# Kernel tuning notes

Measured on AMD Instinct MI355X. Metric: run time of the kernel, lower is better.

The kernel has to match this reference:

```python
import jax, jax.numpy as jnp
import numpy as np

B, S, H, KVH, D, HID = 2, 2048, 32, 8, 128, 4096
WINDOW = 512
EPS = 1e-5
SCALE = D ** -0.5
NEG = jnp.finfo(jnp.float32).min


def cohere_layernorm(x, w):
    # true LayerNorm (mean-subtracting), fp32 compute, weight, no bias
    xf = x.astype(jnp.float32)
    mu = jnp.mean(xf, axis=-1, keepdims=True)
    var = jnp.mean((xf - mu) ** 2, axis=-1, keepdims=True)
    return (w.astype(jnp.float32) * (xf - mu) * jax.lax.rsqrt(var + EPS)).astype(x.dtype)


def rotate_half_interleaved(x):
    # interleaved pairs: (x0,x1,x2,x3,...) -> (-x1,x0,-x3,x2,...)
    x1 = x[..., ::2]
    x2 = x[..., 1::2]
    return jnp.stack([-x2, x1], axis=-1).reshape(x.shape)


def setup_inputs() -> dict:
    key = jax.random.key(0)
    ks = jax.random.split(key, 6)
    hidden_states = jax.random.normal(ks[0], (B, S, HID), jnp.float32)
    position_ids = jnp.broadcast_to(jnp.arange(S, dtype=jnp.int32), (B, S))
    # rotary table with interleave-repeated frequencies (Cohere style)
    inv_freq = 1.0 / (10000.0 ** (jnp.arange(0, D, 2, dtype=jnp.float32) / D))
    freqs = jnp.arange(S, dtype=jnp.float32)[:, None] * inv_freq[None, :]  # [S, D/2]
    emb = jnp.repeat(freqs, 2, axis=-1)  # [S, D]
    cos, sin = jnp.cos(emb), jnp.sin(emb)
    std = 0.02
    # weights stored [in, out] so projection is x @ W
    wq = jax.random.normal(ks[1], (HID, H * D), jnp.float32) * std
    wk = jax.random.normal(ks[2], (HID, KVH * D), jnp.float32) * std
    wv = jax.random.normal(ks[3], (HID, KVH * D), jnp.float32) * std
    wo = jax.random.normal(ks[4], (H * D, HID), jnp.float32) * std
    q_norm_w = jnp.ones((D,), jnp.float32)
    k_norm_w = jnp.ones((D,), jnp.float32)
    return {"hidden_states": hidden_states, "position_ids": position_ids,
            "cos": cos, "sin": sin, "wq": wq, "wk": wk, "wv": wv, "wo": wo,
            "q_norm_w": q_norm_w, "k_norm_w": k_norm_w}


def reference(hidden_states, position_ids, cos, sin, wq, wk, wv, wo, q_norm_w, k_norm_w):
    q = (hidden_states @ wq).reshape(B, S, H, D)
    k = (hidden_states @ wk).reshape(B, S, KVH, D)
    v = (hidden_states @ wv).reshape(B, S, KVH, D)
    # QK LayerNorm over head_dim
    q = cohere_layernorm(q, q_norm_w)
    k = cohere_layernorm(k, k_norm_w)
    # interleaved RoPE; cos/sin gathered by position then broadcast over heads (unsqueeze_dim=2)
    c = cos[position_ids][:, :, None, :]  # [B, S, 1, D]
    s = sin[position_ids][:, :, None, :]
    q = q * c + rotate_half_interleaved(q) * s
    k = k * c + rotate_half_interleaved(k) * s
    # GQA: expand KV heads, attention in bhsd layout
    rep = H // KVH
    qh = jnp.transpose(q, (0, 2, 1, 3))                      # [B, H, S, D]
    kh = jnp.transpose(jnp.repeat(k, rep, axis=2), (0, 2, 1, 3))
    vh = jnp.transpose(jnp.repeat(v, rep, axis=2), (0, 2, 1, 3))
    scores = jnp.einsum('bhqd,bhkd->bhqk', qh, kh) * SCALE   # [B, H, S, S]
    i = jnp.arange(S)[:, None]
    j = jnp.arange(S)[None, :]
    mask = (i >= j) & (i - j < WINDOW)                       # causal + sliding window
    scores = jnp.where(mask[None, None], scores, NEG)
    attn = jax.nn.softmax(scores, axis=-1)
    out = jnp.einsum('bhqk,bhkd->bhqd', attn, vh)
    out = jnp.transpose(out, (0, 2, 1, 3)).reshape(B, S, H * D)
    return out @ wo
```

## Files before the change

kernel.cpp:

```cpp
#include <hip/hip_runtime.h>
#include <hip/hip_bf16.h>
#include <cstdio>
#include <cstdint>

#define B_    2
#define S_    2048
#define H_    32
#define KVH_  8
#define D_    128
#define HID_  4096
#define WIN_  512
#define NROW_ (B_*S_)
#define NKV_  2048
#define SCALE_ 0.08838834764831845f
#define SL2E_  0.12751744932973953f

typedef __attribute__((ext_vector_type(8))) __bf16 bf16x8;
typedef __attribute__((ext_vector_type(4))) __bf16 bf16x4;
typedef __attribute__((ext_vector_type(4))) float  f32x4;

#define GAS __attribute__((address_space(1)))
#define LAS __attribute__((address_space(3)))

__global__ __launch_bounds__(256) void cvt_bf16(const float* __restrict__ in,
                                                __hip_bfloat16* __restrict__ out, int n) {
    int i = (blockIdx.x * 256 + threadIdx.x) * 4;
    if (i >= n) return;
    float4 v = *(const float4*)(in + i);
    __hip_bfloat162 a, b;
    a.x = __float2bfloat16(v.x); a.y = __float2bfloat16(v.y);
    b.x = __float2bfloat16(v.z); b.y = __float2bfloat16(v.w);
    *(__hip_bfloat162*)(out + i)     = a;
    *(__hip_bfloat162*)(out + i + 2) = b;
}

__global__ __launch_bounds__(256) void transpose_cvt(const float* __restrict__ in,
                                                     __hip_bfloat16* __restrict__ out,
                                                     int R, int C) {
    __shared__ float t[32][33];
    int tx = threadIdx.x, ty = threadIdx.y;
    int r0 = blockIdx.y * 32, c0 = blockIdx.x * 32;
    #pragma unroll
    for (int i = 0; i < 4; ++i)
        t[ty + 8*i][tx] = in[(size_t)(r0 + ty + 8*i) * C + c0 + tx];
    __syncthreads();
    #pragma unroll
    for (int i = 0; i < 4; ++i)
        out[(size_t)(c0 + ty + 8*i) * R + r0 + tx] = __float2bfloat16(t[tx][ty + 8*i]);
}

__global__ __launch_bounds__(256) void v_transpose(const float* __restrict__ kvf,
                                                   __hip_bfloat16* __restrict__ vt) {
    __shared__ float t[32][33];
    int tx = threadIdx.x, ty = threadIdx.y;
    int plane = blockIdx.z, b = plane >> 3, g = plane & 7;
    int s0 = blockIdx.x * 32, d0 = blockIdx.y * 32;
    #pragma unroll
    for (int i = 0; i < 4; ++i) {
        int s = s0 + ty + 8*i;
        t[ty + 8*i][tx] = kvf[((size_t)b*S_ + s) * NKV_ + (KVH_*D_) + g*D_ + d0 + tx];
    }
    __syncthreads();
    #pragma unroll
    for (int i = 0; i < 4; ++i) {
        int d = d0 + ty + 8*i;
        vt[(((size_t)b*KVH_ + g) * D_ + d) * S_ + s0 + tx] = __float2bfloat16(t[tx][ty + 8*i]);
    }
}

template <int FN>
__global__ __launch_bounds__(512, 2) void gemm_t(const __hip_bfloat16* __restrict__ A,
                                                 const __hip_bfloat16* __restrict__ Bt,
                                                 float* __restrict__ C,
                                                 int M, int N, int K, int nbx) {
    constexpr int BN   = FN * 64;
    constexpr int SLOT = (256 + BN) * 32;
    constexpr int LPT  = 2 + BN / 128;
    __shared__ __align__(16) __hip_bfloat16 L[4 * SLOT];
    const int tid  = threadIdx.x;
    const int lane = tid & 63, w = tid >> 6;
    const int wm = w >> 2, wn = w & 3;
    const int lc = lane & 15, lg = lane >> 4;
    const int nwg = gridDim.x, cpx = nwg >> 3;
    const int bid = blockIdx.x;
    const int swz = (bid & 7) * cpx + (bid >> 3);
    const int by = swz / nbx, bx = swz - by * nbx;
    const size_t row0 = (size_t)by * 256, col0 = (size_t)bx * BN;
    const int nt = K >> 5;

    const int srow = tid >> 2;
    const int spc  = tid & 3;
    const int slx  = spc ^ ((srow >> 1) & 3);
    const __hip_bfloat16* Ab = A  + row0 * K;
    const __hip_bfloat16* Bb = Bt + col0 * K;

#define STG(tile_) do {                                                                    \
    const int ss_ = (tile_) & 3;                                                           \
    const int kt_ = ((tile_) < nt) ? (tile_) : (nt - 1);  \
    _Pragma("unroll")                                                                      \
    for (int rh_ = 0; rh_ < 2; ++rh_)                                                      \
        __builtin_amdgcn_global_load_lds(                                                  \
            (const GAS void*)(Ab + (size_t)(rh_*128 + srow) * K + kt_*32 + slx*8),         \
            (LAS void*)&L[ss_*SLOT + rh_*4096 + w*512], 16, 0, 0);                         \
    _Pragma("unroll")                                                                      \
    for (int bh_ = 0; bh_ < BN/128; ++bh_)                                                 \
        __builtin_amdgcn_global_load_lds(                                                  \
            (const GAS void*)(Bb + (size_t)(bh_*128 + srow) * K + kt_*32 + slx*8),         \
            (LAS void*)&L[ss_*SLOT + 8192 + bh_*4096 + w*512], 16, 0, 0);                  \
} while (0)

#define VMW() do {                                                                         \
    if constexpr (FN == 4) asm volatile("s_waitcnt vmcnt(8)" ::: "memory");                \
    else                   asm volatile("s_waitcnt vmcnt(6)" ::: "memory");                \
} while (0)

    f32x4 acc[2][4][FN] = {};
    bf16x8 afr[2][4], bfr[FN];

#define PHASE(tt_) do {                                                                    \
    const int s_ = (tt_) & 3;                                                              \
    _Pragma("unroll")                                                                      \
    for (int fn = 0; fn < FN; ++fn) {                                                      \
        const int rB = wn*(FN*16) + fn*16 + lc;                                            \
        bfr[fn] = *(const bf16x8*)&L[s_*SLOT + 8192 + rB*32 + ((lg ^ ((rB >> 1) & 3)) * 8)]; \
    }                                                                                      \
    _Pragma("unroll")                                                                      \
    for (int qm = 0; qm < 2; ++qm)                                                         \
        _Pragma("unroll")                                                                  \
        for (int fm = 0; fm < 4; ++fm) {                                                   \
            const int rA = wm*128 + qm*64 + fm*16 + lc;                                    \
            afr[qm][fm] = *(const bf16x8*)&L[s_*SLOT + rA*32 + ((lg ^ ((rA >> 1) & 3)) * 8)]; \
        }                                                                                  \
    STG((tt_) + 3);                                                                        \
    VMW();                                                                                 \
    asm volatile("s_barrier" ::: "memory");                                                \
    asm volatile("s_waitcnt lgkmcnt(0)" ::: "memory");                                     \
    __builtin_amdgcn_sched_barrier(0);                                                     \
    __builtin_amdgcn_s_setprio(1);                                                         \
    _Pragma("unroll")                                                                      \
    for (int qm = 0; qm < 2; ++qm)                                                         \
        _Pragma("unroll")                                                                  \
        for (int fm = 0; fm < 4; ++fm)                                                     \
            _Pragma("unroll")                                                              \
            for (int fn = 0; fn < FN; ++fn)                                                \
                acc[qm][fm][fn] = __builtin_amdgcn_mfma_f32_16x16x32_bf16(                 \
                    afr[qm][fm], bfr[fn], acc[qm][fm][fn], 0, 0, 0);                       \
    __builtin_amdgcn_s_setprio(0);                                                         \
} while (0)

    STG(0); STG(1); STG(2);
    VMW();
    asm volatile("s_barrier" ::: "memory");

    for (int t = 0; t < nt; t += 2) {
        PHASE(t);
        PHASE(t + 1);
    }
#undef PHASE
#undef STG
#undef VMW
    asm volatile("s_waitcnt vmcnt(0)" ::: "memory");

    #pragma unroll
    for (int qm = 0; qm < 2; ++qm)
        #pragma unroll
        for (int fm = 0; fm < 4; ++fm)
            #pragma unroll
            for (int fn = 0; fn < FN; ++fn) {
                const size_t col = col0 + wn*(FN*16) + fn*16 + lc;
                #pragma unroll
                for (int rr = 0; rr < 4; ++rr) {
                    const size_t row = row0 + wm*128 + qm*64 + fm*16 + lg*4 + rr;
                    C[row * N + col] = acc[qm][fm][fn][rr];
                }
            }
}

template <int NH, int LD, int XOFF>
__global__ __launch_bounds__(256) void ln_rope(const float* __restrict__ x,
                                               const float* __restrict__ wln,
                                               const float* __restrict__ cosT,
                                               const float* __restrict__ sinT,
                                               const int* __restrict__ pids,
                                               __hip_bfloat16* __restrict__ out) {
    const int lane = threadIdx.x & 63, wv = threadIdx.x >> 6;
    const int r = blockIdx.x * 4 + wv;
    const int h = r % NH;
    const int bs = r / NH;
    const int b = bs / S_, s = bs % S_;
    const float2 xv = *(const float2*)(x + (size_t)bs * LD + XOFF + h*D_ + lane*2);
    float sum = xv.x + xv.y;
    #pragma unroll
    for (int o = 32; o; o >>= 1) sum += __shfl_xor(sum, o);
    const float mu = sum * (1.f / D_);
    const float dx = xv.x - mu, dy = xv.y - mu;
    float vs = dx*dx + dy*dy;
    #pragma unroll
    for (int o = 32; o; o >>= 1) vs += __shfl_xor(vs, o);
    const float rs = rsqrtf(vs * (1.f / D_) + 1e-5f);
    const float2 w2 = *(const float2*)(wln + lane*2);
    const float y0 = w2.x * dx * rs, y1 = w2.y * dy * rs;
    const int p = pids[bs];
    const float2 c  = *(const float2*)(cosT + (size_t)p * D_ + lane*2);
    const float2 sn = *(const float2*)(sinT + (size_t)p * D_ + lane*2);
    __hip_bfloat162 ov;
    ov.x = __float2bfloat16(y0 * c.x - y1 * sn.x);
    ov.y = __float2bfloat16(y1 * c.y + y0 * sn.y);
    *(__hip_bfloat162*)(out + (((size_t)b * NH + h) * S_ + s) * D_ + lane*2) = ov;
}

static __device__ __forceinline__ int sigk_(int r) { return (r & 3) | ((r >> 1) & 4); }

__global__ __launch_bounds__(256) void attn_fwd(const __hip_bfloat16* __restrict__ qr,
                                                const __hip_bfloat16* __restrict__ kr,
                                                const __hip_bfloat16* __restrict__ vt,
                                                __hip_bfloat16* __restrict__ ao) {
    __shared__ __align__(16) __hip_bfloat16 Ksl[2][64*D_];
    __shared__ __align__(16) __hip_bfloat16 Vsl[2][D_*64];
    const int lane = threadIdx.x & 63, w = threadIdx.x >> 6;
    const int lq = lane & 15, lg = lane >> 4;
    const int blk = blockIdx.x;
    const int qt = blk >> 6;
    const int bh = blk & 63;
    const int h = bh & (H_-1), b = bh >> 5;
    const int g = h >> 2;
    const int q0 = qt*64 + w*16;
    const int q  = q0 + lq;

    const __hip_bfloat16* qbase = qr + (((size_t)b*H_ + h)*S_ + q0) * D_;
    const __hip_bfloat16* kbase = kr + ((size_t)b*KVH_ + g) * (size_t)S_ * D_;
    const __hip_bfloat16* vbase = vt + ((size_t)b*KVH_ + g) * (size_t)D_ * S_;

    const int srK = lane >> 4, scK = lane & 15;
    const int srV = lane >> 3, scV = lane & 7;

#define STAGE(nb, k0s) do {                                                              \
    _Pragma("unroll")                                                                    \
    for (int s_ = 0; s_ < 4; ++s_) {                                                     \
        const int rK_ = s_*16 + w*4 + srK;                                               \
        const __hip_bfloat16* srcK_ = kbase + (size_t)((k0s) + rK_)*D_                   \
                                      + ((scK ^ sigk_(rK_)) * 8);                        \
        __builtin_amdgcn_global_load_lds((const GAS void*)srcK_,                         \
            (LAS void*)&Ksl[nb][(s_*16 + w*4)*D_], 16, 0, 0);                            \
    }                                                                                    \
    _Pragma("unroll")                                                                    \
    for (int s_ = 0; s_ < 4; ++s_) {                                                     \
        const int dV_ = s_*32 + w*8 + srV;                                               \
        const __hip_bfloat16* srcV_ = vbase + (size_t)dV_*S_ + (k0s)                     \
                                      + ((scV ^ (dV_ & 7)) * 8);                         \
        __builtin_amdgcn_global_load_lds((const GAS void*)srcV_,                         \
            (LAS void*)&Vsl[nb][(s_*32 + w*8)*64], 16, 0, 0);                            \
    }                                                                                    \
} while (0)

    bf16x8 qf[4];
    #pragma unroll
    for (int kk = 0; kk < 4; ++kk)
        qf[kk] = *(const bf16x8*)(qbase + lq*D_ + kk*32 + lg*8);

    f32x4 o[8] = {};
    float m = -1e30f, l = 0.f;

    int kst = qt*64 - (WIN_ - 1); if (kst < 0) kst = 0; kst &= ~63;
    const int nt = qt + 1 - (kst >> 6);
    const int kldrow = 8*(lq >> 2) + (lq & 3);

    STAGE(0, kst);

    for (int t = 0; t < nt; ++t) {
        const int k0 = kst + t*64;
        const int buf = t & 1;
        if (t + 1 < nt) {
            STAGE((t + 1) & 1, k0 + 64);
            asm volatile("s_waitcnt vmcnt(8)" ::: "memory");
        } else {
            asm volatile("s_waitcnt vmcnt(0)" ::: "memory");
        }
        __builtin_amdgcn_s_barrier();

        f32x4 sc[2][2] = {};
        __builtin_amdgcn_s_setprio(1);
        #pragma unroll
        for (int kb = 0; kb < 2; ++kb)
            #pragma unroll
            for (int f = 0; f < 2; ++f) {
                const int rA = kb*32 + 4*f + kldrow;
                const __hip_bfloat16* kp = &Ksl[buf][rA*D_];
                #pragma unroll
                for (int kk = 0; kk < 4; ++kk) {
                    bf16x8 ka = *(const bf16x8*)(kp + (((kk*4 + lg) ^ sigk_(rA)) * 8));
                    sc[kb][f] = __builtin_amdgcn_mfma_f32_16x16x32_bf16(ka, qf[kk], sc[kb][f], 0, 0, 0);
                }
            }
        __builtin_amdgcn_s_setprio(0);

        const int dqk = q - (k0 + 8*lg);
        float pv[16];
        float mx = -INFINITY;
        #pragma unroll
        for (int kb = 0; kb < 2; ++kb)
            #pragma unroll
            for (int f = 0; f < 2; ++f)
                #pragma unroll
                for (int r = 0; r < 4; ++r) {
                    const int c = kb*32 + 4*f + r;
                    const int d = dqk - c;
                    float v = (d >= 0 && d < WIN_) ? sc[kb][f][r] * SL2E_ : -INFINITY;
                    pv[kb*8 + f*4 + r] = v;
                    mx = fmaxf(mx, v);
                }
        mx = fmaxf(mx, __shfl_xor(mx, 16));
        mx = fmaxf(mx, __shfl_xor(mx, 32));
        const float mn = fmaxf(m, mx);
        const float alpha = exp2f(m - mn);
        float ls = 0.f;
        union { bf16x8 v; __hip_bfloat16 e[8]; } pu[2];
        #pragma unroll
        for (int kb = 0; kb < 2; ++kb)
            #pragma unroll
            for (int j = 0; j < 8; ++j) {
                const float p = exp2f(pv[kb*8 + j] - mn);
                ls += p;
                pu[kb].e[j] = __float2bfloat16(p);
            }
        ls += __shfl_xor(ls, 16);
        ls += __shfl_xor(ls, 32);
        l = l * alpha + ls;
        m = mn;
        #pragma unroll
        for (int n = 0; n < 8; ++n) {
            o[n][0] *= alpha; o[n][1] *= alpha; o[n][2] *= alpha; o[n][3] *= alpha;
        }

        __builtin_amdgcn_s_setprio(1);
        #pragma unroll
        for (int kb = 0; kb < 2; ++kb)
            #pragma unroll
            for (int n = 0; n < 8; ++n) {
                const int dR = n*16 + lq;
                bf16x8 vf8 = *(const bf16x8*)(&Vsl[buf][dR*64] + (((kb*4 + lg) ^ (dR & 7)) * 8));
                o[n] = __builtin_amdgcn_mfma_f32_16x16x32_bf16(vf8, pu[kb].v, o[n], 0, 0, 0);
            }
        __builtin_amdgcn_s_setprio(0);

        if (t + 1 < nt) __builtin_amdgcn_s_barrier();
    }
#undef STAGE

    const float rinv = 1.f / l;
    #pragma unroll
    for (int n = 0; n < 8; ++n) {
        union { bf16x4 v; __hip_bfloat16 e[4]; } ov;
        #pragma unroll
        for (int r = 0; r < 4; ++r) ov.e[r] = __float2bfloat16(o[n][r] * rinv);
        *(bf16x4*)(ao + ((size_t)b*S_ + q)*(H_*D_) + h*D_ + n*16 + lg*4) = ov.v;
    }
}

extern "C" void kernel_launch(void* const* d_in, const int* in_sizes, int n_in,
                              void* d_out, int out_size, void* d_ws, size_t ws_size,
                              hipStream_t stream) {
    const float* hidden = (const float*)d_in[0];
    const int*   pids   = (const int*)  d_in[1];
    const float* cosT   = (const float*)d_in[2];
    const float* sinT   = (const float*)d_in[3];
    const float* wq     = (const float*)d_in[4];
    const float* wk     = (const float*)d_in[5];
    const float* wv     = (const float*)d_in[6];
    const float* wo     = (const float*)d_in[7];
    const float* qnw    = (const float*)d_in[8];
    const float* knw    = (const float*)d_in[9];
    float* out = (float*)d_out;

    char* base = (char*)d_ws;
    size_t off = 0;
    auto take = [&](size_t bytes) -> void* {
        void* q = base + off;
        off = (off + bytes + 255) & ~(size_t)255;
        return q;
    };
    float* qf            = (float*)take((size_t)NROW_*HID_*4);
    float* kvf           = (float*)take((size_t)NROW_*NKV_*4);
    __hip_bfloat16* hb   = (__hip_bfloat16*)take((size_t)NROW_*HID_*2);
    __hip_bfloat16* wqT  = (__hip_bfloat16*)take((size_t)HID_*HID_*2);
    __hip_bfloat16* wkvT = (__hip_bfloat16*)take((size_t)NKV_*HID_*2);
    __hip_bfloat16* woT  = (__hip_bfloat16*)take((size_t)HID_*HID_*2);
    __hip_bfloat16* qr   = (__hip_bfloat16*)take((size_t)B_*H_*S_*D_*2);
    __hip_bfloat16* kr   = (__hip_bfloat16*)take((size_t)B_*KVH_*S_*D_*2);
    __hip_bfloat16* vt   = (__hip_bfloat16*)take((size_t)B_*KVH_*S_*D_*2);
    __hip_bfloat16* ao   = (__hip_bfloat16*)qf;

    if (off > ws_size) {
        fprintf(stderr, "WORKSPACE TOO SMALL: need %zu have %zu\n", off, ws_size);
        return;
    }

    cvt_bf16<<<(NROW_*HID_)/1024, 256, 0, stream>>>(hidden, hb, NROW_*HID_);
    transpose_cvt<<<dim3((H_*D_)/32,   HID_/32), dim3(32,8), 0, stream>>>(wq, wqT, HID_, H_*D_);
    transpose_cvt<<<dim3((KVH_*D_)/32, HID_/32), dim3(32,8), 0, stream>>>(wk, wkvT, HID_, KVH_*D_);
    transpose_cvt<<<dim3((KVH_*D_)/32, HID_/32), dim3(32,8), 0, stream>>>(wv, wkvT + (size_t)(KVH_*D_)*HID_, HID_, KVH_*D_);
    transpose_cvt<<<dim3(HID_/32, (H_*D_)/32),   dim3(32,8), 0, stream>>>(wo, woT, H_*D_, HID_);

    gemm_t<4><<<(NROW_/256)*(HID_/256), 512, 0, stream>>>(hb, wqT,  qf,  NROW_, HID_, HID_, HID_/256);
    gemm_t<2><<<(NROW_/256)*(NKV_/128), 512, 0, stream>>>(hb, wkvT, kvf, NROW_, NKV_, HID_, NKV_/128);

    ln_rope<H_,   HID_, 0><<<(B_*S_*H_)/4,   256, 0, stream>>>(qf,  qnw, cosT, sinT, pids, qr);
    ln_rope<KVH_, NKV_, 0><<<(B_*S_*KVH_)/4, 256, 0, stream>>>(kvf, knw, cosT, sinT, pids, kr);
    v_transpose<<<dim3(S_/32, D_/32, B_*KVH_), dim3(32,8), 0, stream>>>(kvf, vt);

    attn_fwd<<<B_*H_*(S_/64), 256, 0, stream>>>(qr, kr, vt, ao);

    gemm_t<4><<<(NROW_/256)*(HID_/256), 512, 0, stream>>>(ao, woT, out, NROW_, HID_, H_*D_, HID_/256);
}
```

Measured before the change: 519.0 us.

## Split GEMM k-step into two half-M phases with interleaved A/B staging

The GEMM main loop is restructured so each k-tile is processed in two halves. A fragments for the first 64 rows are loaded, the A stage for a future tile is issued, and MFMAs run. Then the second-half A fragments are loaded and the B stage is issued. This halves A-fragment register usage and spreads global-to-LDS loads across the iteration to overlap them with MFMA work. In exchange it adds a second barrier per k-step and drops the 2x unroll of the loop. The vmcnt thresholds change because A and B loads are now issued separately, and getting those counts wrong could cause stale LDS reads.

Result: no change. 513.2 us (-1.1%).

```diff
diff --git a/kernel.cpp b/kernel.cpp
--- a/kernel.cpp
+++ b/kernel.cpp
@@ -74,8 +74,8 @@
                                                  float* __restrict__ C,
                                                  int M, int N, int K, int nbx) {
     constexpr int BN   = FN * 64;
+    constexpr int BLD  = BN / 128;
     constexpr int SLOT = (256 + BN) * 32;
-    constexpr int LPT  = 2 + BN / 128;
     __shared__ __align__(16) __hip_bfloat16 L[4 * SLOT];
     const int tid  = threadIdx.x;
     const int lane = tid & 63, w = tid >> 6;
@@ -94,7 +94,7 @@
     const __hip_bfloat16* Ab = A  + row0 * K;
     const __hip_bfloat16* Bb = Bt + col0 * K;
 
-#define STG(tile_) do {                                                                    \
+#define STGA(tile_) do {                                                                   \
     const int ss_ = (tile_) & 3;                                                           \
     const int kt_ = ((tile_) < nt) ? (tile_) : (nt - 1);  \
     _Pragma("unroll")                                                                      \
@@ -102,63 +102,74 @@
         __builtin_amdgcn_global_load_lds(                                                  \
             (const GAS void*)(Ab + (size_t)(rh_*128 + srow) * K + kt_*32 + slx*8),         \
             (LAS void*)&L[ss_*SLOT + rh_*4096 + w*512], 16, 0, 0);                         \
+} while (0)
+
+#define STGB(tile_) do {                                                                   \
+    const int ss_ = (tile_) & 3;                                                           \
+    const int kt_ = ((tile_) < nt) ? (tile_) : (nt - 1);                                   \
     _Pragma("unroll")                                                                      \
-    for (int bh_ = 0; bh_ < BN/128; ++bh_)                                                 \
+    for (int bh_ = 0; bh_ < BLD; ++bh_)                                                    \
         __builtin_amdgcn_global_load_lds(                                                  \
             (const GAS void*)(Bb + (size_t)(bh_*128 + srow) * K + kt_*32 + slx*8),         \
             (LAS void*)&L[ss_*SLOT + 8192 + bh_*4096 + w*512], 16, 0, 0);                  \
 } while (0)
 
-#define VMW() do {                                                                         \
-    if constexpr (FN == 4) asm volatile("s_waitcnt vmcnt(8)" ::: "memory");                \
-    else                   asm volatile("s_waitcnt vmcnt(6)" ::: "memory");                \
-} while (0)
-
     f32x4 acc[2][4][FN] = {};
-    bf16x8 afr[2][4], bfr[FN];
-
-#define PHASE(tt_) do {                                                                    \
-    const int s_ = (tt_) & 3;                                                              \
-    _Pragma("unroll")                                                                      \
-    for (int fn = 0; fn < FN; ++fn) {                                                      \
-        const int rB = wn*(FN*16) + fn*16 + lc;                                            \
-        bfr[fn] = *(const bf16x8*)&L[s_*SLOT + 8192 + rB*32 + ((lg ^ ((rB >> 1) & 3)) * 8)]; \
-    }                                                                                      \
-    _Pragma("unroll")                                                                      \
-    for (int qm = 0; qm < 2; ++qm)                                                         \
-        _Pragma("unroll")                                                                  \
-        for (int fm = 0; fm < 4; ++fm) {                                                   \
-            const int rA = wm*128 + qm*64 + fm*16 + lc;                                    \
-            afr[qm][fm] = *(const bf16x8*)&L[s_*SLOT + rA*32 + ((lg ^ ((rA >> 1) & 3)) * 8)]; \
-        }                                                                                  \
-    STG((tt_) + 3);                                                                        \
-    VMW();                                                                                 \
-    asm volatile("s_barrier" ::: "memory");                                                \
-    asm volatile("s_waitcnt lgkmcnt(0)" ::: "memory");                                     \
-    __builtin_amdgcn_sched_barrier(0);                                                     \
-    __builtin_amdgcn_s_setprio(1);                                                         \
-    _Pragma("unroll")                                                                      \
-    for (int qm = 0; qm < 2; ++qm)                                                         \
-        _Pragma("unroll")                                                                  \
-        for (int fm = 0; fm < 4; ++fm)                                                     \
-            _Pragma("unroll")                                                              \
-            for (int fn = 0; fn < FN; ++fn)                                                \
-                acc[qm][fm][fn] = __builtin_amdgcn_mfma_f32_16x16x32_bf16(                 \
-                    afr[qm][fm], bfr[fn], acc[qm][fm][fn], 0, 0, 0);                       \
-    __builtin_amdgcn_s_setprio(0);                                                         \
-} while (0)
-
-    STG(0); STG(1); STG(2);
-    VMW();
+    bf16x8 afr[4], bfr[FN];
+
+    STGA(0); STGB(0); STGA(1); STGB(1); STGA(2); STGB(2);
+    if constexpr (FN == 4) asm volatile("s_waitcnt vmcnt(8)" ::: "memory");
+    else                   asm volatile("s_waitcnt vmcnt(6)" ::: "memory");
     asm volatile("s_barrier" ::: "memory");
 
-    for (int t = 0; t < nt; t += 2) {
-        PHASE(t);
-        PHASE(t + 1);
-    }
-#undef PHASE
-#undef STG
-#undef VMW
+    for (int t = 0; t < nt; ++t) {
+        const int s_ = t & 3;
+
+        #pragma unroll
+        for (int fn = 0; fn < FN; ++fn) {
+            const int rB = wn*(FN*16) + fn*16 + lc;
+            bfr[fn] = *(const bf16x8*)&L[s_*SLOT + 8192 + rB*32 + ((lg ^ ((rB >> 1) & 3)) * 8)];
+        }
+        #pragma unroll
+        for (int fm = 0; fm < 4; ++fm) {
+            const int rA = wm*128 + fm*16 + lc;
+            afr[fm] = *(const bf16x8*)&L[s_*SLOT + rA*32 + ((lg ^ ((rA >> 1) & 3)) * 8)];
+        }
+        STGA(t + 3);
+        if constexpr (FN == 4) asm volatile("s_waitcnt vmcnt(10)" ::: "memory");
+        else                   asm volatile("s_waitcnt vmcnt(8)"  ::: "memory");
+        asm volatile("s_barrier" ::: "memory");
+        asm volatile("s_waitcnt lgkmcnt(0)" ::: "memory");
+        __builtin_amdgcn_sched_barrier(0);
+        __builtin_amdgcn_s_setprio(1);
+        #pragma unroll
+        for (int fm = 0; fm < 4; ++fm)
+            #pragma unroll
+            for (int fn = 0; fn < FN; ++fn)
+                acc[0][fm][fn] = __builtin_amdgcn_mfma_f32_16x16x32_bf16(
+                    afr[fm], bfr[fn], acc[0][fm][fn], 0, 0, 0);
+        __builtin_amdgcn_s_setprio(0);
+
+        #pragma unroll
+        for (int fm = 0; fm < 4; ++fm) {
+            const int rA = wm*128 + 64 + fm*16 + lc;
+            afr[fm] = *(const bf16x8*)&L[s_*SLOT + rA*32 + ((lg ^ ((rA >> 1) & 3)) * 8)];
+        }
+        STGB(t + 3);
+        asm volatile("s_waitcnt lgkmcnt(0)" ::: "memory");
+        __builtin_amdgcn_sched_barrier(0);
+        __builtin_amdgcn_s_setprio(1);
+        #pragma unroll
+        for (int fm = 0; fm < 4; ++fm)
+            #pragma unroll
+            for (int fn = 0; fn < FN; ++fn)
+                acc[1][fm][fn] = __builtin_amdgcn_mfma_f32_16x16x32_bf16(
+                    afr[fm], bfr[fn], acc[1][fm][fn], 0, 0, 0);
+        __builtin_amdgcn_s_setprio(0);
+        asm volatile("s_barrier" ::: "memory");
+    }
+#undef STGA
+#undef STGB
     asm volatile("s_waitcnt vmcnt(0)" ::: "memory");
 
     #pragma unroll
```
